# Kernel tuning notes

Measured on AMD Instinct MI355X. Metric: run time of the kernel, lower is better.

## Reference

```python
import jax, jax.numpy as jnp
import numpy as np

H_DIM = 4096
N_HEADS = 4
D_HEAD = H_DIM // N_HEADS  # 1024; also forced to equal the node count N
N = D_HEAD
LN_EPS = 1e-5


def setup_inputs() -> dict:
    key = jax.random.key(0)
    ks = jax.random.split(key, 10)
    s = 0.02
    return {
        "node1": jax.random.normal(ks[0], (N, H_DIM), dtype=jnp.float32),
        "node2": jax.random.normal(ks[1], (N, H_DIM), dtype=jnp.float32),
        # stacked per-head projection weights (torch Linear y = x @ W^T + b; here W stored as [h, in, out])
        "Wq": jax.random.normal(ks[2], (N_HEADS, H_DIM, D_HEAD), dtype=jnp.float32) * s,
        "bq": jax.random.normal(ks[3], (N_HEADS, D_HEAD), dtype=jnp.float32) * s,
        "Wk": jax.random.normal(ks[4], (N_HEADS, H_DIM, D_HEAD), dtype=jnp.float32) * s,
        "bk": jax.random.normal(ks[5], (N_HEADS, D_HEAD), dtype=jnp.float32) * s,
        "Wv": jax.random.normal(ks[6], (N_HEADS, H_DIM, D_HEAD), dtype=jnp.float32) * s,
        "bv": jax.random.normal(ks[7], (N_HEADS, D_HEAD), dtype=jnp.float32) * s,
        "gamma": jnp.ones((H_DIM,), dtype=jnp.float32),
        "beta": jnp.zeros((H_DIM,), dtype=jnp.float32),
    }


def reference(node1, node2, Wq, bq, Wk, bk, Wv, bv, gamma, beta):
    # per-head projections: [h, N, d]
    q = jnp.einsum('nd,hdf->hnf', node1, Wq) + bq[:, None, :]
    k = jnp.einsum('md,hdf->hmf', node2, Wk) + bk[:, None, :]
    v = jnp.einsum('md,hdf->hmf', node2, Wv) + bv[:, None, :]
    scale = 1.0 / jnp.sqrt(jnp.asarray(D_HEAD, dtype=q.dtype))
    # scores [h, N, N]; elementwise-multiplied by v (no softmax). Valid because N == D_HEAD.
    r = (jnp.einsum('hnf,hmf->hnm', q, k) * scale) * v
    # concat heads along last dim: [N, h * d] = [N, H_DIM]
    out = jnp.transpose(r, (1, 0, 2)).reshape(N, H_DIM)
    # LayerNorm over last dim (biased variance, matching torch)
    mu = jnp.mean(out, axis=-1, keepdims=True)
    var = jnp.mean((out - mu) ** 2, axis=-1, keepdims=True)
    return (out - mu) * jax.lax.rsqrt(var + LN_EPS) * gamma + beta
```

## Files before the change

kernel.cpp:

```cpp
#include <hip/hip_runtime.h>

#define H_DIM 4096
#define DH 1024
#define NROWS 1024

typedef __attribute__((ext_vector_type(8))) short short8;
typedef __attribute__((ext_vector_type(4))) short short4v;
typedef __attribute__((ext_vector_type(4))) float f32x4;

#define AS_GLOBAL __attribute__((address_space(1)))
#define AS_LDS __attribute__((address_space(3)))

__device__ __forceinline__ short f2bf(float f) {
  union { float f; unsigned u; } v; v.f = f;
  unsigned r = v.u + 0x7fffu + ((v.u >> 16) & 1u);
  return (short)(r >> 16);
}
__device__ __forceinline__ float bf2f(short s) {
  union { unsigned u; float f; } v;
  v.u = ((unsigned)(unsigned short)s) << 16;
  return v.f;
}

__device__ __forceinline__ void gload16(const void* g, void* l) {
  __builtin_amdgcn_global_load_lds((const AS_GLOBAL void*)g, (AS_LDS void*)l, 16, 0, 0);
}

__global__ void convert_nodes(const float* __restrict__ n1, const float* __restrict__ n2,
                              short* __restrict__ o1, short* __restrict__ o2) {
  const float* src = blockIdx.y ? n2 : n1;
  short* dst = blockIdx.y ? o2 : o1;
  const size_t i = ((size_t)blockIdx.x * 256 + threadIdx.x) * 8;
  f32x4 a = *(const f32x4*)&src[i];
  f32x4 b = *(const f32x4*)&src[i + 4];
  short8 s;
  s[0] = f2bf(a.x); s[1] = f2bf(a.y); s[2] = f2bf(a.z); s[3] = f2bf(a.w);
  s[4] = f2bf(b.x); s[5] = f2bf(b.y); s[6] = f2bf(b.z); s[7] = f2bf(b.w);
  *(short8*)&dst[i] = s;
}

__global__ void convert_w_all(const float* __restrict__ Wq, const float* __restrict__ Wk,
                              const float* __restrict__ Wv, short* __restrict__ Wt) {
  __shared__ short tile[64][72];
  const int z = blockIdx.z, dt = blockIdx.y, ft = blockIdx.x;
  const float* W = (z < 4) ? Wq : (z < 8) ? Wk : Wv;
  const int h = z & 3;
  const float* Wh = W + (size_t)h * H_DIM * DH;
  short* Wth = Wt + (size_t)z * DH * H_DIM;
  const int t = threadIdx.x;
  {
    const int d = t >> 2, f0 = (t & 3) * 16;
    const float* src = Wh + (size_t)(dt * 64 + d) * DH + ft * 64 + f0;
    f32x4 v0 = *(const f32x4*)(src + 0);
    f32x4 v1 = *(const f32x4*)(src + 4);
    f32x4 v2 = *(const f32x4*)(src + 8);
    f32x4 v3 = *(const f32x4*)(src + 12);
    short8 s0, s1;
    s0[0] = f2bf(v0.x); s0[1] = f2bf(v0.y); s0[2] = f2bf(v0.z); s0[3] = f2bf(v0.w);
    s0[4] = f2bf(v1.x); s0[5] = f2bf(v1.y); s0[6] = f2bf(v1.z); s0[7] = f2bf(v1.w);
    s1[0] = f2bf(v2.x); s1[1] = f2bf(v2.y); s1[2] = f2bf(v2.z); s1[3] = f2bf(v2.w);
    s1[4] = f2bf(v3.x); s1[5] = f2bf(v3.y); s1[6] = f2bf(v3.z); s1[7] = f2bf(v3.w);
    *(short8*)&tile[d][f0] = s0;
    *(short8*)&tile[d][f0 + 8] = s1;
  }
  __syncthreads();
  {
    const int f = t >> 2, d0 = (t & 3) * 16;
    short8 o0, o1;
#pragma unroll
    for (int j = 0; j < 8; ++j) o0[j] = tile[d0 + j][f];
#pragma unroll
    for (int j = 0; j < 8; ++j) o1[j] = tile[d0 + 8 + j][f];
    short* dst = Wth + (size_t)(ft * 64 + f) * H_DIM + dt * 64 + d0;
    *(short8*)(dst) = o0;
    *(short8*)(dst + 8) = o1;
  }
}

#define BAR __builtin_amdgcn_s_barrier();
#define WAITL { asm volatile("s_waitcnt lgkmcnt(0)" ::: "memory"); __builtin_amdgcn_sched_barrier(0); }
#define PRIO1 __builtin_amdgcn_s_setprio(1);
#define PRIO0 __builtin_amdgcn_s_setprio(0);

#define STG(isA, slab, ktn) \
  gload16(((isA) ? Ag : Bg) + (size_t)(slab) * 64 * H_DIM + (ktn) * 64, \
          smb + ((isA) ? 0 : 65536) + ((ktn) & 1) * 32768 + (slab) * 8192 + wub)

#define DSA(mh, cbuf) { _Pragma("unroll") for (int mp = 0; mp < 4; ++mp) { \
    const int rrow = wm * 128 + (mh) * 64 + mp * 16 + lr; \
    const char* pb = smb + (cbuf) * 32768 + rrow * 128; \
    af[mp * 2 + 0] = *(const short8*)(pb + sA0); \
    af[mp * 2 + 1] = *(const short8*)(pb + sA1); } }

#define DSB(nh, cbuf, dst) { _Pragma("unroll") for (int np = 0; np < 2; ++np) { \
    const int brow = wn * 64 + (nh) * 32 + np * 16 + lr; \
    const char* pb = smb + 65536 + (cbuf) * 32768 + brow * 128; \
    dst[np * 2 + 0] = *(const short8*)(pb + sA0); \
    dst[np * 2 + 1] = *(const short8*)(pb + sA1); } }

#define MFMA16(mh, nh, bfr) { _Pragma("unroll") for (int mp = 0; mp < 4; ++mp) \
    { _Pragma("unroll") for (int np = 0; np < 2; ++np) { \
      acc[(mh) * 4 + mp][(nh) * 2 + np] = __builtin_amdgcn_mfma_f32_16x16x32_bf16( \
          af[mp * 2 + 0], bfr[np * 2 + 0], acc[(mh) * 4 + mp][(nh) * 2 + np], 0, 0, 0); \
      acc[(mh) * 4 + mp][(nh) * 2 + np] = __builtin_amdgcn_mfma_f32_16x16x32_bf16( \
          af[mp * 2 + 1], bfr[np * 2 + 1], acc[(mh) * 4 + mp][(nh) * 2 + np], 0, 0, 0); } } }

__launch_bounds__(512, 2)
__global__ void qkv_8p(const short* __restrict__ n1b, const short* __restrict__ n2b,
                       const short* __restrict__ Wt,
                       const float* __restrict__ bq, const float* __restrict__ bk,
                       const float* __restrict__ bv,
                       short* __restrict__ qkv_out) {
  __shared__ short smem[65536];
  char* smb = (char*)smem;

  const int bid = blockIdx.x;
  const int v = (bid & 7) * 24 + (bid >> 3);
  const int gemm = v >> 4;
  const int rr = v & 15;
  const int mt = rr & 3, nt = rr >> 2;
  const int bm0 = mt * 256, bn0 = nt * 256;
  const short* A = (gemm < 4) ? n1b : n2b;
  const short* B = Wt + ((size_t)gemm << 22);
  const float* bias = ((gemm < 4) ? bq : (gemm < 8) ? bk : bv) + (gemm & 3) * DH;
  short* C = qkv_out + ((size_t)gemm << 20);

  const int t = threadIdx.x;
  const int lane = t & 63, w = t >> 6;
  const int wm = w >> 2, wn = w & 3;
  const int lr = lane & 15, lk = lane >> 4;
  const int xorv = lr & 7;
  const int sA0 = (lk ^ xorv) * 16;
  const int sA1 = ((4 + lk) ^ xorv) * 16;

  const int rowA = t >> 3;
  const int sL = (t & 7) ^ (rowA & 7);
  const size_t wub = (size_t)w * 1024;
  const short* Ag = A + (size_t)(bm0 + rowA) * H_DIM + sL * 8;
  const short* Bg = B + (size_t)(bn0 + rowA) * H_DIM + sL * 8;

  f32x4 acc[8][4];
#pragma unroll
  for (int m = 0; m < 8; ++m)
#pragma unroll
    for (int n = 0; n < 4; ++n)
      acc[m][n] = (f32x4)(0.0f);

  short8 af[8], bf0[4], bf1[4];

#pragma unroll
  for (int i = 0; i < 4; ++i) { STG(1, i, 0); }
#pragma unroll
  for (int i = 0; i < 4; ++i) { STG(0, i, 0); }
#pragma unroll
  for (int i = 0; i < 4; ++i) { STG(1, i, 1); }
#pragma unroll
  for (int i = 0; i < 4; ++i) { STG(0, i, 1); }
  asm volatile("s_waitcnt vmcnt(8)" ::: "memory");
  BAR

  const int NKT = H_DIM / 64;
  for (int kt = 0; kt < NKT; ++kt) {
    const int cb = kt & 1;
    const int dost = (kt + 2 < NKT);
    DSA(0, cb)
    DSB(0, cb, bf0)
    BAR
    WAITL
    PRIO1 MFMA16(0, 0, bf0) PRIO0
    BAR
    DSB(1, cb, bf1)
    if (dost) { STG(1, 0, kt + 2); STG(1, 2, kt + 2); }
    BAR
    WAITL
    PRIO1 MFMA16(0, 1, bf1) PRIO0
    BAR
    DSA(1, cb)
    if (dost) { STG(0, 0, kt + 2); STG(0, 1, kt + 2); }
    BAR
    WAITL
    PRIO1 MFMA16(1, 1, bf1) PRIO0
    BAR
    if (dost) { STG(0, 2, kt + 2); STG(0, 3, kt + 2); STG(1, 1, kt + 2); STG(1, 3, kt + 2); }
    PRIO1 MFMA16(1, 0, bf0) PRIO0
    if (dost)               { asm volatile("s_waitcnt vmcnt(8)" ::: "memory"); }
    else if (kt + 1 < NKT)  { asm volatile("s_waitcnt vmcnt(0)" ::: "memory"); }
    BAR
  }

  float bvv[4];
#pragma unroll
  for (int n = 0; n < 4; ++n) bvv[n] = bias[bn0 + wn * 64 + n * 16 + lr];
#pragma unroll
  for (int m = 0; m < 8; ++m) {
    const int row0 = bm0 + wm * 128 + m * 16 + lk * 4;
#pragma unroll
    for (int n = 0; n < 4; ++n) {
      const int col = bn0 + wn * 64 + n * 16 + lr;
#pragma unroll
      for (int e = 0; e < 4; ++e)
        C[(size_t)(row0 + e) * DH + col] = f2bf(acc[m][n][e] + bvv[n]);
    }
  }
}

__device__ __forceinline__ void stage_tile(const short* Xrow0, size_t rowstride, int kbase,
                                           short* lds, int t) {
  const int w = t >> 6;
#pragma unroll
  for (int p = 0; p < 2; ++p) {
    const short* g = Xrow0 + (size_t)(p * 64 + (t >> 2)) * rowstride + kbase + (t & 3) * 8;
    char* l = (char*)lds + p * 4096 + w * 1024;
    gload16(g, l);
  }
}

__launch_bounds__(256)
__global__ void attn_bt(const short* __restrict__ qkv, float* __restrict__ out) {
  const int bid = blockIdx.x;
  const int h = bid >> 6;
  const int tile = bid & 63;
  const short* Q = qkv + (size_t)h * NROWS * DH;
  const short* K = qkv + (size_t)(4 + h) * NROWS * DH;
  const short* V = qkv + (size_t)(8 + h) * NROWS * DH;
  const int bm0 = (tile >> 3) * 128, bn0 = (tile & 7) * 128;

  __shared__ short As[2][4096];
  __shared__ short Bs[2][4096];

  const int t = threadIdx.x;
  const int lane = t & 63, w = t >> 6;
  const int wm = (w >> 1) * 64, wn = (w & 1) * 64;
  const int lr = lane & 15, lk = lane >> 4;

  const short* Arow0 = Q + (size_t)bm0 * DH;
  const short* Brow0 = K + (size_t)bn0 * DH;

  f32x4 acc[4][4];
#pragma unroll
  for (int m = 0; m < 4; ++m)
#pragma unroll
    for (int n = 0; n < 4; ++n)
      acc[m][n] = (f32x4)(0.0f);

  stage_tile(Arow0, DH, 0, &As[0][0], t);
  stage_tile(Brow0, DH, 0, &Bs[0][0], t);
  __syncthreads();

  const int NKT = DH / 32;
  int cur = 0;
  for (int kt = 0; kt < NKT; ++kt) {
    if (kt + 1 < NKT) {
      stage_tile(Arow0, DH, (kt + 1) * 32, &As[cur ^ 1][0], t);
      stage_tile(Brow0, DH, (kt + 1) * 32, &Bs[cur ^ 1][0], t);
    }
    short8 af[4], bf_[4];
#pragma unroll
    for (int m = 0; m < 4; ++m)
      af[m] = *(const short8*)((const char*)&As[cur][0] + (wm + m * 16 + lr) * 64 + lk * 16);
#pragma unroll
    for (int n = 0; n < 4; ++n)
      bf_[n] = *(const short8*)((const char*)&Bs[cur][0] + (wn + n * 16 + lr) * 64 + lk * 16);
#pragma unroll
    for (int m = 0; m < 4; ++m)
#pragma unroll
      for (int n = 0; n < 4; ++n)
        acc[m][n] = __builtin_amdgcn_mfma_f32_16x16x32_bf16(af[m], bf_[n], acc[m][n], 0, 0, 0);
    __syncthreads();
    cur ^= 1;
  }

  const float scale = 0.03125f;
#pragma unroll
  for (int n = 0; n < 4; ++n) {
    const int col = bn0 + wn + n * 16 + lr;
#pragma unroll
    for (int m = 0; m < 4; ++m) {
      const int row0 = bm0 + wm + m * 16 + lk * 4;
#pragma unroll
      for (int r = 0; r < 4; ++r) {
        const int row = row0 + r;
        const float vv = bf2f(V[(size_t)row * DH + col]);
        out[(size_t)row * H_DIM + h * DH + col] = acc[m][n][r] * scale * vv;
      }
    }
  }
}

__launch_bounds__(256, 2)
__global__ void qkv_gemm(const float* __restrict__ node1,
                         const float* __restrict__ node2,
                         const float* __restrict__ Wq, const float* __restrict__ bq,
                         const float* __restrict__ Wk, const float* __restrict__ bk,
                         const float* __restrict__ Wv, const float* __restrict__ bv,
                         short* __restrict__ qkv_out) {
  const int gid = blockIdx.x;
  const int gemm = gid >> 6;
  const int tile = gid & 63;
  const int qkv = gemm >> 2;
  const int h = gemm & 3;
  const float* A = (qkv == 0) ? node1 : node2;
  const float* W = (qkv == 0) ? Wq : (qkv == 1 ? Wk : Wv);
  const float* bias = (qkv == 0) ? bq : (qkv == 1 ? bk : bv);
  const float* B = W + (size_t)h * H_DIM * DH;
  const float* bh = bias + h * DH;
  short* C = qkv_out + (size_t)gemm * NROWS * DH;
  const int bm0 = (tile >> 3) * 128;
  const int bn0 = (tile & 7) * 128;
  __shared__ short As[128][40];
  __shared__ short Bs[128][40];
  const int t = threadIdx.x;
  const int lane = t & 63;
  const int w = t >> 6;
  const int wm = (w >> 1) * 64;
  const int wn = (w & 1) * 64;
  const int lr = lane & 15;
  const int lk = lane >> 4;
  const int ar = t >> 3;
  const int ac = (t & 7) * 4;
  const int bfc = t & 127;
  const int bd = (t >> 7) * 16;
  f32x4 acc[4][4];
#pragma unroll
  for (int m = 0; m < 4; ++m)
#pragma unroll
    for (int n = 0; n < 4; ++n)
      acc[m][n] = (f32x4)(0.0f);
  f32x4 rA[4];
  float rB[16];
  const float* Abase = A + (size_t)bm0 * H_DIM;
  const float* Bbase = B + bn0 + bfc;
#pragma unroll
  for (int p = 0; p < 4; ++p)
    rA[p] = *(const f32x4*)&Abase[(size_t)(ar + 32 * p) * H_DIM + ac];
#pragma unroll
  for (int i = 0; i < 16; ++i)
    rB[i] = Bbase[(size_t)(bd + i) * DH];
  const int NKT = H_DIM / 32;
  for (int kt = 0; kt < NKT; ++kt) {
    __syncthreads();
#pragma unroll
    for (int p = 0; p < 4; ++p) {
      short4v s;
      s.x = f2bf(rA[p].x); s.y = f2bf(rA[p].y);
      s.z = f2bf(rA[p].z); s.w = f2bf(rA[p].w);
      *(short4v*)&As[ar + 32 * p][ac] = s;
    }
    {
      short8 lo, hi;
#pragma unroll
      for (int i = 0; i < 8; ++i) { lo[i] = f2bf(rB[i]); hi[i] = f2bf(rB[8 + i]); }
      *(short8*)&Bs[bfc][bd] = lo;
      *(short8*)&Bs[bfc][bd + 8] = hi;
    }
    __syncthreads();
    if (kt + 1 < NKT) {
      const int k0 = (kt + 1) * 32;
#pragma unroll
      for (int p = 0; p < 4; ++p)
        rA[p] = *(const f32x4*)&Abase[(size_t)(ar + 32 * p) * H_DIM + k0 + ac];
#pragma unroll
      for (int i = 0; i < 16; ++i)
        rB[i] = Bbase[(size_t)(k0 + bd + i) * DH];
    }
    short8 af[4], bf_[4];
#pragma unroll
    for (int m = 0; m < 4; ++m)
      af[m] = *(const short8*)&As[wm + m * 16 + lr][lk * 8];
#pragma unroll
    for (int n = 0; n < 4; ++n)
      bf_[n] = *(const short8*)&Bs[wn + n * 16 + lr][lk * 8];
#pragma unroll
    for (int m = 0; m < 4; ++m)
#pragma unroll
      for (int n = 0; n < 4; ++n)
        acc[m][n] = __builtin_amdgcn_mfma_f32_16x16x32_bf16(af[m], bf_[n], acc[m][n], 0, 0, 0);
  }
#pragma unroll
  for (int n = 0; n < 4; ++n) {
    const int col = bn0 + wn + n * 16 + lr;
    const float bv_ = bh[col];
#pragma unroll
    for (int m = 0; m < 4; ++m) {
      const int row0 = bm0 + wm + m * 16 + lk * 4;
#pragma unroll
      for (int r = 0; r < 4; ++r)
        C[(size_t)(row0 + r) * DH + col] = f2bf(acc[m][n][r] + bv_);
    }
  }
}

__launch_bounds__(256, 4)
__global__ void ln_kernel(float* __restrict__ out, const float* __restrict__ gamma,
                          const float* __restrict__ beta) {
  const int row = blockIdx.x;
  const int t = threadIdx.x;
  float* p = out + (size_t)row * H_DIM;
  f32x4 x[4];
  float s1 = 0.f, s2 = 0.f;
#pragma unroll
  for (int i = 0; i < 4; ++i) {
    x[i] = *(const f32x4*)&p[t * 4 + i * 1024];
    s1 += x[i].x + x[i].y + x[i].z + x[i].w;
    s2 += x[i].x * x[i].x + x[i].y * x[i].y + x[i].z * x[i].z + x[i].w * x[i].w;
  }
#pragma unroll
  for (int o = 32; o > 0; o >>= 1) {
    s1 += __shfl_down(s1, o);
    s2 += __shfl_down(s2, o);
  }
  __shared__ float w1[4], w2[4];
  if ((t & 63) == 0) { w1[t >> 6] = s1; w2[t >> 6] = s2; }
  __syncthreads();
  const float tot1 = w1[0] + w1[1] + w1[2] + w1[3];
  const float tot2 = w2[0] + w2[1] + w2[2] + w2[3];
  const float mu = tot1 * (1.0f / H_DIM);
  const float var = tot2 * (1.0f / H_DIM) - mu * mu;
  const float rs = rsqrtf(var + 1e-5f);
#pragma unroll
  for (int i = 0; i < 4; ++i) {
    const int c = t * 4 + i * 1024;
    const f32x4 g = *(const f32x4*)&gamma[c];
    const f32x4 b = *(const f32x4*)&beta[c];
    f32x4 y;
    y.x = (x[i].x - mu) * rs * g.x + b.x;
    y.y = (x[i].y - mu) * rs * g.y + b.y;
    y.z = (x[i].z - mu) * rs * g.z + b.z;
    y.w = (x[i].w - mu) * rs * g.w + b.w;
    *(f32x4*)&p[c] = y;
  }
}

extern "C" void kernel_launch(void* const* d_in, const int* in_sizes, int n_in,
                              void* d_out, int out_size, void* d_ws, size_t ws_size,
                              hipStream_t stream) {
  const float* node1 = (const float*)d_in[0];
  const float* node2 = (const float*)d_in[1];
  const float* Wq = (const float*)d_in[2];
  const float* bq = (const float*)d_in[3];
  const float* Wk = (const float*)d_in[4];
  const float* bk = (const float*)d_in[5];
  const float* Wv = (const float*)d_in[6];
  const float* bv = (const float*)d_in[7];
  const float* gamma = (const float*)d_in[8];
  const float* beta = (const float*)d_in[9];
  float* out = (float*)d_out;

  const size_t MB = (size_t)1 << 20;
  short* qkv = (short*)d_ws;
  short* n1b = qkv + ((size_t)12 << 20);
  short* n2b = n1b + ((size_t)4 << 20);
  short* Wt = qkv + ((size_t)20 << 20);

  if (ws_size >= 136 * MB) {
    convert_nodes<<<dim3(2048, 2), 256, 0, stream>>>(node1, node2, n1b, n2b);
    convert_w_all<<<dim3(16, 64, 12), 256, 0, stream>>>(Wq, Wk, Wv, Wt);
    qkv_8p<<<192, 512, 0, stream>>>(n1b, n2b, Wt, bq, bk, bv, qkv);
  } else {
    qkv_gemm<<<768, 256, 0, stream>>>(node1, node2, Wq, bq, Wk, bk, Wv, bv, qkv);
  }

  attn_bt<<<256, 256, 0, stream>>>(qkv, out);
  ln_kernel<<<1024, 256, 0, stream>>>(out, gamma, beta);
}
```

Before: 200.4 us.

## Fuse weight fp32-to-bf16 conversion and transpose into QKV GEMM B-tile loads

Removes the separate convert_w_all pass, which transposed and converted all 12 fp32 weight matrices to a bf16 workspace. The GEMM now loads fp32 weight columns straight into registers, converts them with the HIP bf16 intrinsic and writes swizzled bf16 tiles into LDS inside the pipelined k-loop. This drops a full read-write pass over 192 MB of weights and shrinks the workspace requirement. In exchange, the B loads become strided scalar fp32 global reads (8 per row with stride DH) that use many more registers and VMEM instructions, and the waitcnt accounting is changed.

```diff
diff --git a/kernel.cpp b/kernel.cpp
--- a/kernel.cpp
+++ b/kernel.cpp
@@ -1,4 +1,5 @@
 #include <hip/hip_runtime.h>
+#include <hip/hip_bf16.h>
 
 #define H_DIM 4096
 #define DH 1024
@@ -15,6 +16,10 @@
   union { float f; unsigned u; } v; v.f = f;
   unsigned r = v.u + 0x7fffu + ((v.u >> 16) & 1u);
   return (short)(r >> 16);
+}
+__device__ __forceinline__ short bfc(float f) {
+  __hip_bfloat16 h = __float2bfloat16(f);
+  return *(short*)&h;
 }
 __device__ __forceinline__ float bf2f(short s) {
   union { unsigned u; float f; } v;
@@ -39,52 +44,14 @@
   *(short8*)&dst[i] = s;
 }
 
-__global__ void convert_w_all(const float* __restrict__ Wq, const float* __restrict__ Wk,
-                              const float* __restrict__ Wv, short* __restrict__ Wt) {
-  __shared__ short tile[64][72];
-  const int z = blockIdx.z, dt = blockIdx.y, ft = blockIdx.x;
-  const float* W = (z < 4) ? Wq : (z < 8) ? Wk : Wv;
-  const int h = z & 3;
-  const float* Wh = W + (size_t)h * H_DIM * DH;
-  short* Wth = Wt + (size_t)z * DH * H_DIM;
-  const int t = threadIdx.x;
-  {
-    const int d = t >> 2, f0 = (t & 3) * 16;
-    const float* src = Wh + (size_t)(dt * 64 + d) * DH + ft * 64 + f0;
-    f32x4 v0 = *(const f32x4*)(src + 0);
-    f32x4 v1 = *(const f32x4*)(src + 4);
-    f32x4 v2 = *(const f32x4*)(src + 8);
-    f32x4 v3 = *(const f32x4*)(src + 12);
-    short8 s0, s1;
-    s0[0] = f2bf(v0.x); s0[1] = f2bf(v0.y); s0[2] = f2bf(v0.z); s0[3] = f2bf(v0.w);
-    s0[4] = f2bf(v1.x); s0[5] = f2bf(v1.y); s0[6] = f2bf(v1.z); s0[7] = f2bf(v1.w);
-    s1[0] = f2bf(v2.x); s1[1] = f2bf(v2.y); s1[2] = f2bf(v2.z); s1[3] = f2bf(v2.w);
-    s1[4] = f2bf(v3.x); s1[5] = f2bf(v3.y); s1[6] = f2bf(v3.z); s1[7] = f2bf(v3.w);
-    *(short8*)&tile[d][f0] = s0;
-    *(short8*)&tile[d][f0 + 8] = s1;
-  }
-  __syncthreads();
-  {
-    const int f = t >> 2, d0 = (t & 3) * 16;
-    short8 o0, o1;
-#pragma unroll
-    for (int j = 0; j < 8; ++j) o0[j] = tile[d0 + j][f];
-#pragma unroll
-    for (int j = 0; j < 8; ++j) o1[j] = tile[d0 + 8 + j][f];
-    short* dst = Wth + (size_t)(ft * 64 + f) * H_DIM + dt * 64 + d0;
-    *(short8*)(dst) = o0;
-    *(short8*)(dst + 8) = o1;
-  }
-}
-
 #define BAR __builtin_amdgcn_s_barrier();
 #define WAITL { asm volatile("s_waitcnt lgkmcnt(0)" ::: "memory"); __builtin_amdgcn_sched_barrier(0); }
 #define PRIO1 __builtin_amdgcn_s_setprio(1);
 #define PRIO0 __builtin_amdgcn_s_setprio(0);
 
-#define STG(isA, slab, ktn) \
-  gload16(((isA) ? Ag : Bg) + (size_t)(slab) * 64 * H_DIM + (ktn) * 64, \
-          smb + ((isA) ? 0 : 65536) + ((ktn) & 1) * 32768 + (slab) * 8192 + wub)
+#define STGA(slab, ktn) \
+  gload16(Ag + (size_t)(slab) * 64 * H_DIM + (ktn) * 64, \
+          smb + ((ktn) & 1) * 32768 + (slab) * 8192 + wub)
 
 #define DSA(mh, cbuf) { _Pragma("unroll") for (int mp = 0; mp < 4; ++mp) { \
     const int rrow = wm * 128 + (mh) * 64 + mp * 16 + lr; \
@@ -105,12 +72,25 @@
       acc[(mh) * 4 + mp][(nh) * 2 + np] = __builtin_amdgcn_mfma_f32_16x16x32_bf16( \
           af[mp * 2 + 1], bfr[np * 2 + 1], acc[(mh) * 4 + mp][(nh) * 2 + np], 0, 0, 0); } } }
 
+#define BLOAD(ktn) { _Pragma("unroll") for (int i = 0; i < 4; ++i) { \
+    const float* wp = Wg_base + (size_t)((ktn) * 64 + (bslg_ + i) * 8) * DH; \
+    _Pragma("unroll") for (int j = 0; j < 8; ++j) \
+      wr[i][j] = wp[(size_t)j * DH]; } }
+
+#define BWRITE(ktn) { \
+    char* bb = smb + 65536 + ((ktn) & 1) * 32768 + brow_ * 128; \
+    _Pragma("unroll") for (int i = 0; i < 4; ++i) { \
+      short8 cvv; \
+      _Pragma("unroll") for (int j = 0; j < 8; ++j) cvv[j] = bfc(wr[i][j]); \
+      *(short8*)(bb + ((bslg_ + i) ^ (brow_ & 7)) * 16) = cvv; } }
+
 __launch_bounds__(512, 2)
-__global__ void qkv_8p(const short* __restrict__ n1b, const short* __restrict__ n2b,
-                       const short* __restrict__ Wt,
-                       const float* __restrict__ bq, const float* __restrict__ bk,
-                       const float* __restrict__ bv,
-                       short* __restrict__ qkv_out) {
+__global__ void qkv_f(const short* __restrict__ n1b, const short* __restrict__ n2b,
+                      const float* __restrict__ Wq, const float* __restrict__ Wk,
+                      const float* __restrict__ Wv,
+                      const float* __restrict__ bq, const float* __restrict__ bk,
+                      const float* __restrict__ bv,
+                      short* __restrict__ qkv_out) {
   __shared__ short smem[65536];
   char* smb = (char*)smem;
 
@@ -121,7 +101,8 @@
   const int mt = rr & 3, nt = rr >> 2;
   const int bm0 = mt * 256, bn0 = nt * 256;
   const short* A = (gemm < 4) ? n1b : n2b;
-  const short* B = Wt + ((size_t)gemm << 22);
+  const float* Wsrc = (gemm < 4) ? Wq : (gemm < 8) ? Wk : Wv;
+  const float* Wg = Wsrc + (size_t)(gemm & 3) * H_DIM * DH;
   const float* bias = ((gemm < 4) ? bq : (gemm < 8) ? bk : bv) + (gemm & 3) * DH;
   short* C = qkv_out + ((size_t)gemm << 20);
 
@@ -137,7 +118,11 @@
   const int sL = (t & 7) ^ (rowA & 7);
   const size_t wub = (size_t)w * 1024;
   const short* Ag = A + (size_t)(bm0 + rowA) * H_DIM + sL * 8;
-  const short* Bg = B + (size_t)(bn0 + rowA) * H_DIM + sL * 8;
+
+  const int brow_ = t & 255;
+  const int bslg_ = (t >> 8) * 4;
+  const float* Wg_base = Wg + bn0 + brow_;
+  float wr[4][8];
 
   f32x4 acc[8][4];
 #pragma unroll
@@ -148,21 +133,23 @@
 
   short8 af[8], bf0[4], bf1[4];
 
-#pragma unroll
-  for (int i = 0; i < 4; ++i) { STG(1, i, 0); }
-#pragma unroll
-  for (int i = 0; i < 4; ++i) { STG(0, i, 0); }
-#pragma unroll
-  for (int i = 0; i < 4; ++i) { STG(1, i, 1); }
-#pragma unroll
-  for (int i = 0; i < 4; ++i) { STG(0, i, 1); }
-  asm volatile("s_waitcnt vmcnt(8)" ::: "memory");
+  BLOAD(0)
+  BWRITE(0)
+  BLOAD(1)
+  BWRITE(1)
+#pragma unroll
+  for (int i = 0; i < 4; ++i) { STGA(i, 0); }
+#pragma unroll
+  for (int i = 0; i < 4; ++i) { STGA(i, 1); }
+  asm volatile("s_waitcnt vmcnt(4)" ::: "memory");
+  WAITL
   BAR
 
   const int NKT = H_DIM / 64;
   for (int kt = 0; kt < NKT; ++kt) {
     const int cb = kt & 1;
     const int dost = (kt + 2 < NKT);
+    if (dost) { BLOAD(kt + 2) }
     DSA(0, cb)
     DSB(0, cb, bf0)
     BAR
@@ -170,20 +157,20 @@
     PRIO1 MFMA16(0, 0, bf0) PRIO0
     BAR
     DSB(1, cb, bf1)
-    if (dost) { STG(1, 0, kt + 2); STG(1, 2, kt + 2); }
+    if (dost) { STGA(0, kt + 2); STGA(2, kt + 2); }
     BAR
     WAITL
     PRIO1 MFMA16(0, 1, bf1) PRIO0
     BAR
     DSA(1, cb)
-    if (dost) { STG(0, 0, kt + 2); STG(0, 1, kt + 2); }
+    if (dost) { BWRITE(kt + 2) }
     BAR
     WAITL
     PRIO1 MFMA16(1, 1, bf1) PRIO0
     BAR
-    if (dost) { STG(0, 2, kt + 2); STG(0, 3, kt + 2); STG(1, 1, kt + 2); STG(1, 3, kt + 2); }
+    if (dost) { STGA(1, kt + 2); STGA(3, kt + 2); }
     PRIO1 MFMA16(1, 0, bf0) PRIO0
-    if (dost)               { asm volatile("s_waitcnt vmcnt(8)" ::: "memory"); }
+    if (dost)               { asm volatile("s_waitcnt vmcnt(4)" ::: "memory"); }
     else if (kt + 1 < NKT)  { asm volatile("s_waitcnt vmcnt(0)" ::: "memory"); }
     BAR
   }
@@ -318,7 +305,7 @@
   const int lk = lane >> 4;
   const int ar = t >> 3;
   const int ac = (t & 7) * 4;
-  const int bfc = t & 127;
+  const int bfcX = t & 127;
   const int bd = (t >> 7) * 16;
   f32x4 acc[4][4];
 #pragma unroll
@@ -329,7 +316,7 @@
   f32x4 rA[4];
   float rB[16];
   const float* Abase = A + (size_t)bm0 * H_DIM;
-  const float* Bbase = B + bn0 + bfc;
+  const float* Bbase = B + bn0 + bfcX;
 #pragma unroll
   for (int p = 0; p < 4; ++p)
     rA[p] = *(const f32x4*)&Abase[(size_t)(ar + 32 * p) * H_DIM + ac];
@@ -350,8 +337,8 @@
       short8 lo, hi;
 #pragma unroll
       for (int i = 0; i < 8; ++i) { lo[i] = f2bf(rB[i]); hi[i] = f2bf(rB[8 + i]); }
-      *(short8*)&Bs[bfc][bd] = lo;
-      *(short8*)&Bs[bfc][bd + 8] = hi;
+      *(short8*)&Bs[bfcX][bd] = lo;
+      *(short8*)&Bs[bfcX][bd + 8] = hi;
     }
     __syncthreads();
     if (kt + 1 < NKT) {
@@ -450,12 +437,10 @@
   short* qkv = (short*)d_ws;
   short* n1b = qkv + ((size_t)12 << 20);
   short* n2b = n1b + ((size_t)4 << 20);
-  short* Wt = qkv + ((size_t)20 << 20);
-
-  if (ws_size >= 136 * MB) {
+
+  if (ws_size >= 40 * MB) {
     convert_nodes<<<dim3(2048, 2), 256, 0, stream>>>(node1, node2, n1b, n2b);
-    convert_w_all<<<dim3(16, 64, 12), 256, 0, stream>>>(Wq, Wk, Wv, Wt);
-    qkv_8p<<<192, 512, 0, stream>>>(n1b, n2b, Wt, bq, bk, bv, qkv);
+    qkv_f<<<192, 512, 0, stream>>>(n1b, n2b, Wq, Wk, Wv, bq, bk, bv, qkv);
   } else {
     qkv_gemm<<<768, 256, 0, stream>>>(node1, node2, Wq, bq, Wk, bk, Wv, bv, qkv);
   }
```

New measurement: 203.1 us. No clear change (+1.3%).
